# Kernel optimization log

Measured on AMD Instinct MI355X. Metric: run time of the kernel, lower is better.

The kernel has to match this reference:

```python
import jax, jax.numpy as jnp
import numpy as np

B, L, K = 8, 512, 30
F = 128          # node_feat_dim
P = 32           # pair_feat_dim
ED = P + 1       # edge_feat_dim = pair_feat_dim + 1 (rel_dist appended)
NL = 4           # num_layers
H = 128          # hidden_dim


def setup_inputs() -> dict:
    key = jax.random.key(0)
    ks = jax.random.split(key, 14)
    R = jax.random.normal(ks[0], (B, L, 3, 3), dtype=jnp.float32)
    t = jax.random.normal(ks[1], (B, L, 3), dtype=jnp.float32) * 10.0  # spread-out CA coords
    res_feat = jax.random.normal(ks[2], (B, L, F), dtype=jnp.float32)
    pair_feat = jax.random.normal(ks[3], (B, L, L, P), dtype=jnp.float32)
    mask_res = jax.random.bernoulli(ks[4], 0.9, (B, L))
    cin = 2 * F + ED + 1   # coord_net input dim
    nin = F + ED           # node_net input dim
    u = lambda k_, shp, fan: jax.random.uniform(k_, shp, jnp.float32, -1.0 / np.sqrt(fan), 1.0 / np.sqrt(fan))
    return {
        "R": R, "t": t, "res_feat": res_feat, "pair_feat": pair_feat, "mask_res": mask_res,
        "coord_w1": u(ks[5], (NL, cin, H), cin), "coord_b1": u(ks[6], (NL, H), cin),
        "coord_w2": u(ks[7], (NL, H, 1), H),    "coord_b2": u(ks[8], (NL, 1), H),
        "node_w1": u(ks[9], (NL, nin, H), nin), "node_b1": u(ks[10], (NL, H), nin),
        "node_w2": u(ks[11], (NL, H, F), H),    "node_b2": u(ks[12], (NL, F), H),
    }


def reference(R, t, res_feat, pair_feat, mask_res,
              coord_w1, coord_b1, coord_w2, coord_b2,
              node_w1, node_b1, node_w2, node_b2):
    Bv, Lv = mask_res.shape
    pos3 = t.reshape(Bv, Lv, 3)

    # --- KNN graph per batch element (k nearest, no self-loops) ---
    sq = jnp.sum(pos3 * pos3, axis=-1)                                   # [B,L]
    d2 = sq[:, :, None] + sq[:, None, :] - 2.0 * jnp.einsum('bid,bjd->bij', pos3, pos3)
    d2 = d2 + jnp.eye(Lv, dtype=d2.dtype) * 1e10                          # exclude self-loop
    _, nbr_local = jax.lax.top_k(-d2, K)                                  # [B,L,K] neighbor (src) indices per center (dst)
    nbr_global = (nbr_local + (jnp.arange(Bv) * Lv)[:, None, None]).reshape(Bv * Lv, K)

    # --- fixed edge attributes: pair_feat[b, src, dst] ++ initial rel_dist ---
    bi = jnp.arange(Bv)[:, None, None]
    ci = jnp.arange(Lv)[None, :, None]
    epf = pair_feat[bi, nbr_local, ci].reshape(Bv * Lv, K, P)             # [N,K,P]
    pflat = pos3.reshape(-1, 3)
    rel0 = pflat[nbr_global] - pflat[:, None, :]
    dist0 = jnp.linalg.norm(rel0, axis=-1, keepdims=True)                 # [N,K,1]
    edge_attr = jnp.concatenate([epf, dist0], axis=-1)                    # [N,K,ED]

    # constant degree K per node => scatter_mean(dst) == mean over K axis
    agg_edge = edge_attr.mean(axis=1)                                     # [N,ED]
    mflat = mask_res.reshape(-1)
    valid = (mflat[nbr_global] & mflat[:, None]).astype(edge_attr.dtype)[..., None]  # [N,K,1]

    x = res_feat.reshape(Bv * Lv, -1)
    p = pflat
    for l in range(coord_w1.shape[0]):
        rel = p[:, None, :] - p[nbr_global]                               # pos[dst]-pos[src], [N,K,3]
        rd = jnp.linalg.norm(rel, axis=-1, keepdims=True)
        xs = x[nbr_global]                                                # x[src]
        xd = jnp.broadcast_to(x[:, None, :], xs.shape)                    # x[dst]
        cf = jnp.concatenate([xs, xd, edge_attr, rd], axis=-1)            # [N,K,2F+ED+1]
        h = jax.nn.relu(cf @ coord_w1[l] + coord_b1[l])
        w = h @ coord_w2[l] + coord_b2[l]                                 # [N,K,1]
        p = p + (w * rel * valid).mean(axis=1)                            # scatter_mean of delta_coord
        nf = jnp.concatenate([x, agg_edge], axis=-1)
        x = jax.nn.relu(nf @ node_w1[l] + node_b1[l]) @ node_w2[l] + node_b2[l]
    return x.reshape(Bv, Lv, -1)
```

## Files before the change

kernel.cpp:

```cpp
#include <hip/hip_runtime.h>
#include <math.h>

#define LSEQ 512
#define KNN 30
#define NNODES 4096

__device__ float g_agg[NNODES * 33];

__device__ __forceinline__ unsigned long long shfl_xor_u64(unsigned long long v, int m) {
  unsigned lo = (unsigned)__shfl_xor((int)(unsigned)(v & 0xFFFFFFFFull), m, 64);
  unsigned hi = (unsigned)__shfl_xor((int)(unsigned)(v >> 32), m, 64);
  return ((unsigned long long)hi << 32) | lo;
}

__global__ __launch_bounds__(256) void knn_agg_kernel(
    const float* __restrict__ t, const float* __restrict__ pair_feat) {
  __shared__ float sx[LSEQ], sy[LSEQ], sz[LSEQ], sq[LSEQ];
  __shared__ int nbr[4][KNN];
  const int blk = blockIdx.x;
  const int tid = threadIdx.x;
  const int b = blk >> 7;
  for (int j = tid; j < LSEQ; j += 256) {
    float x = t[(b * LSEQ + j) * 3 + 0];
    float y = t[(b * LSEQ + j) * 3 + 1];
    float z = t[(b * LSEQ + j) * 3 + 2];
    sx[j] = x; sy[j] = y; sz[j] = z;
    sq[j] = x * x + y * y + z * z;
  }
  __syncthreads();
  const int w = tid >> 6;
  const int lane = tid & 63;
  const int i = blk * 4 + w;
  const int il = i & (LSEQ - 1);
  const float xi = sx[il], yi = sy[il], zi = sz[il], sqi = sq[il];

  unsigned long long k64[8];
#pragma unroll
  for (int m = 0; m < 8; ++m) {
    int j = lane + 64 * m;
    float d2 = sqi + sq[j] - 2.0f * (xi * sx[j] + yi * sy[j] + zi * sz[j]);
    if (j == il) d2 = 1e30f;
    unsigned u = __float_as_uint(d2);
    u = (u & 0x80000000u) ? ~u : (u | 0x80000000u);
    k64[m] = ((unsigned long long)u << 32) | (unsigned)j;
  }
  unsigned long long lbest = k64[0];
#pragma unroll
  for (int m = 1; m < 8; ++m) lbest = (k64[m] < lbest) ? k64[m] : lbest;

  for (int it = 0; it < KNN; ++it) {
    unsigned long long v = lbest;
#pragma unroll
    for (int off = 32; off >= 1; off >>= 1) {
      unsigned long long o = shfl_xor_u64(v, off);
      v = (o < v) ? o : v;
    }
    int jwin = (int)(v & 0xFFFFFFFFull);
    if (lane == it) nbr[w][it] = jwin;
    if ((jwin & 63) == lane) {
      k64[jwin >> 6] = ~0ull;
      lbest = k64[0];
#pragma unroll
      for (int m = 1; m < 8; ++m) lbest = (k64[m] < lbest) ? k64[m] : lbest;
    }
  }

  float acc = 0.0f;
  const int half = lane >> 5;
  const int c = lane & 31;
  const int base_b = b * LSEQ;
#pragma unroll
  for (int itr = 0; itr < KNN / 2; ++itr) {
    int k = itr * 2 + half;
    int j = nbr[w][k];
    acc += pair_feat[((base_b + j) * LSEQ + il) * 32 + c];
  }
  float other = __shfl_xor(acc, 32, 64);
  float tot = acc + other;
  if (lane < 32) g_agg[i * 33 + c] = tot * (1.0f / KNN);

  float dval = 0.0f;
  if (lane < KNN) {
    int j = nbr[w][lane];
    float dx = xi - sx[j], dy = yi - sy[j], dz = zi - sz[j];
    dval = sqrtf(dx * dx + dy * dy + dz * dz);
  }
#pragma unroll
  for (int off = 32; off >= 1; off >>= 1) dval += __shfl_xor(dval, off, 64);
  if (lane == 0) g_agg[i * 33 + 32] = dval * (1.0f / KNN);
}

#define MT 16
#define NFS 196
#define HS 132
#define WSS 132

__global__ __launch_bounds__(256) void node_mlp_kernel(
    const float* __restrict__ res_feat,
    const float* __restrict__ w1, const float* __restrict__ b1,
    const float* __restrict__ w2, const float* __restrict__ b2,
    float* __restrict__ out) {
  __shared__ float nf[MT * NFS];
  __shared__ float hb[MT * HS];
  __shared__ float wbuf[32 * WSS];
  const int tid = threadIdx.x;
  const int node0 = blockIdx.x * MT;
  const int tx = tid & 31, ty = tid >> 5;
  const int c0 = tx * 4, r0 = ty * 2;

#pragma unroll
  for (int q = 0; q < 2; ++q) {
    int f4 = tid + 256 * q;
    int r = f4 >> 5, c4 = f4 & 31;
    *(float4*)&nf[r * NFS + c4 * 4] =
        *(const float4*)&res_feat[(node0 + r) * 128 + c4 * 4];
  }
  for (int idx = tid; idx < MT * 33; idx += 256) {
    int r = idx / 33, cc = idx - r * 33;
    nf[r * NFS + 128 + cc] = g_agg[(node0 + r) * 33 + cc];
  }
  for (int idx = tid; idx < MT * 31; idx += 256) {
    int r = idx / 31, cc = idx - r * 31;
    nf[r * NFS + 161 + cc] = 0.0f;
  }
  __syncthreads();

  for (int l = 0; l < 4; ++l) {
    const float* W1 = w1 + l * 161 * 128;
    float4 acc[2];
    float4 bin = *(const float4*)&b1[l * 128 + c0];
#pragma unroll
    for (int ii = 0; ii < 2; ++ii) acc[ii] = bin;
    for (int kc = 0; kc < 6; ++kc) {
      __syncthreads();
#pragma unroll
      for (int q = 0; q < 4; ++q) {
        int f4 = tid + 256 * q;
        int kk = f4 >> 5, c4 = f4 & 31;
        int row = kc * 32 + kk;
        row = row > 160 ? 160 : row;
        *(float4*)&wbuf[kk * WSS + c4 * 4] = *(const float4*)&W1[row * 128 + c4 * 4];
      }
      __syncthreads();
#pragma unroll
      for (int k4 = 0; k4 < 8; ++k4) {
        float4 av[2], wv[4];
#pragma unroll
        for (int ii = 0; ii < 2; ++ii)
          av[ii] = *(const float4*)&nf[(r0 + ii) * NFS + kc * 32 + k4 * 4];
#pragma unroll
        for (int q = 0; q < 4; ++q)
          wv[q] = *(const float4*)&wbuf[(k4 * 4 + q) * WSS + c0];
#pragma unroll
        for (int ii = 0; ii < 2; ++ii) {
          const float* ap = (const float*)&av[ii];
#pragma unroll
          for (int q = 0; q < 4; ++q) {
            acc[ii].x = fmaf(ap[q], wv[q].x, acc[ii].x);
            acc[ii].y = fmaf(ap[q], wv[q].y, acc[ii].y);
            acc[ii].z = fmaf(ap[q], wv[q].z, acc[ii].z);
            acc[ii].w = fmaf(ap[q], wv[q].w, acc[ii].w);
          }
        }
      }
    }
#pragma unroll
    for (int ii = 0; ii < 2; ++ii) {
      float4 v = acc[ii];
      v.x = fmaxf(v.x, 0.0f); v.y = fmaxf(v.y, 0.0f);
      v.z = fmaxf(v.z, 0.0f); v.w = fmaxf(v.w, 0.0f);
      *(float4*)&hb[(r0 + ii) * HS + c0] = v;
    }

    const float* W2 = w2 + l * 128 * 128;
    float4 acc2[2];
    float4 bin2 = *(const float4*)&b2[l * 128 + c0];
#pragma unroll
    for (int ii = 0; ii < 2; ++ii) acc2[ii] = bin2;
    for (int kc = 0; kc < 4; ++kc) {
      __syncthreads();
#pragma unroll
      for (int q = 0; q < 4; ++q) {
        int f4 = tid + 256 * q;
        int kk = f4 >> 5, c4 = f4 & 31;
        int row = kc * 32 + kk;
        *(float4*)&wbuf[kk * WSS + c4 * 4] = *(const float4*)&W2[row * 128 + c4 * 4];
      }
      __syncthreads();
#pragma unroll
      for (int k4 = 0; k4 < 8; ++k4) {
        float4 av[2], wv[4];
#pragma unroll
        for (int ii = 0; ii < 2; ++ii)
          av[ii] = *(const float4*)&hb[(r0 + ii) * HS + kc * 32 + k4 * 4];
#pragma unroll
        for (int q = 0; q < 4; ++q)
          wv[q] = *(const float4*)&wbuf[(k4 * 4 + q) * WSS + c0];
#pragma unroll
        for (int ii = 0; ii < 2; ++ii) {
          const float* ap = (const float*)&av[ii];
#pragma unroll
          for (int q = 0; q < 4; ++q) {
            acc2[ii].x = fmaf(ap[q], wv[q].x, acc2[ii].x);
            acc2[ii].y = fmaf(ap[q], wv[q].y, acc2[ii].y);
            acc2[ii].z = fmaf(ap[q], wv[q].z, acc2[ii].z);
            acc2[ii].w = fmaf(ap[q], wv[q].w, acc2[ii].w);
          }
        }
      }
    }
    if (l < 3) {
#pragma unroll
      for (int ii = 0; ii < 2; ++ii)
        *(float4*)&nf[(r0 + ii) * NFS + c0] = acc2[ii];
    } else {
#pragma unroll
      for (int ii = 0; ii < 2; ++ii)
        *(float4*)&out[(node0 + r0 + ii) * 128 + c0] = acc2[ii];
    }
  }
}

extern "C" void kernel_launch(void* const* d_in, const int* in_sizes, int n_in,
                              void* d_out, int out_size, void* d_ws, size_t ws_size,
                              hipStream_t stream) {
  const float* t         = (const float*)d_in[1];
  const float* res_feat  = (const float*)d_in[2];
  const float* pair_feat = (const float*)d_in[3];
  const float* nw1       = (const float*)d_in[9];
  const float* nb1       = (const float*)d_in[10];
  const float* nw2       = (const float*)d_in[11];
  const float* nb2       = (const float*)d_in[12];
  float* out = (float*)d_out;
  (void)in_sizes; (void)n_in; (void)out_size; (void)d_ws; (void)ws_size;

  knn_agg_kernel<<<1024, 256, 0, stream>>>(t, pair_feat);
  node_mlp_kernel<<<NNODES / MT, 256, 0, stream>>>(res_feat, nw1, nb1, nw2, nb2, out);
}
```

Baseline: 419.8 us.

## Use DPP wave reduction in KNN and prefetch weight chunks in node MLP

The KNN argmin reduction swaps the xor-shuffle butterfly for DPP row shifts plus row_bcast, then reads the result from lane 63. The node MLP drops to 128 threads with 4 rows per thread. It register-prefetches the next 32-row weight chunk across both layers' GEMMs, and handles weight row 160 with a separate fma instead of a padded sixth chunk. This aims to cut reduction latency, global-load stalls and wasted padded work, at the cost of more registers and fewer threads per block.

```diff
diff --git a/kernel.cpp b/kernel.cpp
--- a/kernel.cpp
+++ b/kernel.cpp
@@ -7,10 +7,14 @@
 
 __device__ float g_agg[NNODES * 33];
 
-__device__ __forceinline__ unsigned long long shfl_xor_u64(unsigned long long v, int m) {
-  unsigned lo = (unsigned)__shfl_xor((int)(unsigned)(v & 0xFFFFFFFFull), m, 64);
-  unsigned hi = (unsigned)__shfl_xor((int)(unsigned)(v >> 32), m, 64);
-  return ((unsigned long long)hi << 32) | lo;
+template <int CTRL>
+__device__ __forceinline__ unsigned long long dpp_min(unsigned long long v) {
+  int lo = (int)(unsigned)(v & 0xFFFFFFFFull);
+  int hi = (int)(unsigned)(v >> 32);
+  int plo = __builtin_amdgcn_update_dpp(lo, lo, CTRL, 0xF, 0xF, false);
+  int phi = __builtin_amdgcn_update_dpp(hi, hi, CTRL, 0xF, 0xF, false);
+  unsigned long long o = ((unsigned long long)(unsigned)phi << 32) | (unsigned)plo;
+  return (o < v) ? o : v;
 }
 
 __global__ __launch_bounds__(256) void knn_agg_kernel(
@@ -50,13 +54,14 @@
 
   for (int it = 0; it < KNN; ++it) {
     unsigned long long v = lbest;
-#pragma unroll
-    for (int off = 32; off >= 1; off >>= 1) {
-      unsigned long long o = shfl_xor_u64(v, off);
-      v = (o < v) ? o : v;
-    }
-    int jwin = (int)(v & 0xFFFFFFFFull);
-    if (lane == it) nbr[w][it] = jwin;
+    v = dpp_min<0x111>(v);
+    v = dpp_min<0x112>(v);
+    v = dpp_min<0x114>(v);
+    v = dpp_min<0x118>(v);
+    v = dpp_min<0x142>(v);
+    v = dpp_min<0x143>(v);
+    int jwin = __builtin_amdgcn_readlane((int)(unsigned)(v & 0xFFFFFFFFull), 63);
+    if (lane == 0) nbr[w][it] = jwin;
     if ((jwin & 63) == lane) {
       k64[jwin >> 6] = ~0ull;
       lbest = k64[0];
@@ -91,11 +96,12 @@
 }
 
 #define MT 16
-#define NFS 196
+#define NFS 164
 #define HS 132
 #define WSS 132
-
-__global__ __launch_bounds__(256) void node_mlp_kernel(
+#define NCHUNK 36
+
+__global__ __launch_bounds__(128) void node_mlp_kernel(
     const float* __restrict__ res_feat,
     const float* __restrict__ w1, const float* __restrict__ b1,
     const float* __restrict__ w2, const float* __restrict__ b2,
@@ -106,53 +112,72 @@
   const int tid = threadIdx.x;
   const int node0 = blockIdx.x * MT;
   const int tx = tid & 31, ty = tid >> 5;
-  const int c0 = tx * 4, r0 = ty * 2;
-
-#pragma unroll
-  for (int q = 0; q < 2; ++q) {
-    int f4 = tid + 256 * q;
+  const int c0 = tx * 4, r0 = ty * 4;
+
+#pragma unroll
+  for (int q = 0; q < 4; ++q) {
+    int f4 = tid + 128 * q;
     int r = f4 >> 5, c4 = f4 & 31;
     *(float4*)&nf[r * NFS + c4 * 4] =
         *(const float4*)&res_feat[(node0 + r) * 128 + c4 * 4];
   }
-  for (int idx = tid; idx < MT * 33; idx += 256) {
+  for (int idx = tid; idx < MT * 33; idx += 128) {
     int r = idx / 33, cc = idx - r * 33;
     nf[r * NFS + 128 + cc] = g_agg[(node0 + r) * 33 + cc];
   }
-  for (int idx = tid; idx < MT * 31; idx += 256) {
-    int r = idx / 31, cc = idx - r * 31;
-    nf[r * NFS + 161 + cc] = 0.0f;
-  }
-  __syncthreads();
-
+
+  auto chunk_ptr = [&](int g) -> const float* {
+    int l = g / 9, r = g - l * 9;
+    return (r < 5) ? (w1 + (l * 161 + r * 32) * 128)
+                   : (w2 + (l * 128 + (r - 5) * 32) * 128);
+  };
+  float4 pre[8];
+  {
+    const float* cp = chunk_ptr(0);
+#pragma unroll
+    for (int q = 0; q < 8; ++q) {
+      int f4 = tid + 128 * q;
+      pre[q] = *(const float4*)&cp[(f4 >> 5) * 128 + (f4 & 31) * 4];
+    }
+  }
+
+  int g = 0;
   for (int l = 0; l < 4; ++l) {
-    const float* W1 = w1 + l * 161 * 128;
-    float4 acc[2];
-    float4 bin = *(const float4*)&b1[l * 128 + c0];
-#pragma unroll
-    for (int ii = 0; ii < 2; ++ii) acc[ii] = bin;
-    for (int kc = 0; kc < 6; ++kc) {
-      __syncthreads();
-#pragma unroll
-      for (int q = 0; q < 4; ++q) {
-        int f4 = tid + 256 * q;
-        int kk = f4 >> 5, c4 = f4 & 31;
-        int row = kc * 32 + kk;
-        row = row > 160 ? 160 : row;
-        *(float4*)&wbuf[kk * WSS + c4 * 4] = *(const float4*)&W1[row * 128 + c4 * 4];
+    float4 w160 = *(const float4*)&w1[(l * 161 + 160) * 128 + c0];
+
+    float4 acc[4];
+    {
+      float4 bin = *(const float4*)&b1[l * 128 + c0];
+#pragma unroll
+      for (int ii = 0; ii < 4; ++ii) acc[ii] = bin;
+    }
+    for (int kc = 0; kc < 5; ++kc, ++g) {
+      __syncthreads();
+#pragma unroll
+      for (int q = 0; q < 8; ++q) {
+        int f4 = tid + 128 * q;
+        *(float4*)&wbuf[(f4 >> 5) * WSS + (f4 & 31) * 4] = pre[q];
+      }
+      if (g + 1 < NCHUNK) {
+        const float* cp = chunk_ptr(g + 1);
+#pragma unroll
+        for (int q = 0; q < 8; ++q) {
+          int f4 = tid + 128 * q;
+          pre[q] = *(const float4*)&cp[(f4 >> 5) * 128 + (f4 & 31) * 4];
+        }
       }
       __syncthreads();
 #pragma unroll
       for (int k4 = 0; k4 < 8; ++k4) {
-        float4 av[2], wv[4];
-#pragma unroll
-        for (int ii = 0; ii < 2; ++ii)
+        float4 av[4], wv[4];
+#pragma unroll
+        for (int ii = 0; ii < 4; ++ii)
           av[ii] = *(const float4*)&nf[(r0 + ii) * NFS + kc * 32 + k4 * 4];
 #pragma unroll
         for (int q = 0; q < 4; ++q)
           wv[q] = *(const float4*)&wbuf[(k4 * 4 + q) * WSS + c0];
 #pragma unroll
-        for (int ii = 0; ii < 2; ++ii) {
+        for (int ii = 0; ii < 4; ++ii) {
           const float* ap = (const float*)&av[ii];
 #pragma unroll
           for (int q = 0; q < 4; ++q) {
@@ -165,39 +190,49 @@
       }
     }
 #pragma unroll
-    for (int ii = 0; ii < 2; ++ii) {
+    for (int ii = 0; ii < 4; ++ii) {
+      float a160 = nf[(r0 + ii) * NFS + 160];
       float4 v = acc[ii];
-      v.x = fmaxf(v.x, 0.0f); v.y = fmaxf(v.y, 0.0f);
-      v.z = fmaxf(v.z, 0.0f); v.w = fmaxf(v.w, 0.0f);
+      v.x = fmaxf(fmaf(a160, w160.x, v.x), 0.0f);
+      v.y = fmaxf(fmaf(a160, w160.y, v.y), 0.0f);
+      v.z = fmaxf(fmaf(a160, w160.z, v.z), 0.0f);
+      v.w = fmaxf(fmaf(a160, w160.w, v.w), 0.0f);
       *(float4*)&hb[(r0 + ii) * HS + c0] = v;
     }
 
-    const float* W2 = w2 + l * 128 * 128;
-    float4 acc2[2];
-    float4 bin2 = *(const float4*)&b2[l * 128 + c0];
-#pragma unroll
-    for (int ii = 0; ii < 2; ++ii) acc2[ii] = bin2;
-    for (int kc = 0; kc < 4; ++kc) {
-      __syncthreads();
-#pragma unroll
-      for (int q = 0; q < 4; ++q) {
-        int f4 = tid + 256 * q;
-        int kk = f4 >> 5, c4 = f4 & 31;
-        int row = kc * 32 + kk;
-        *(float4*)&wbuf[kk * WSS + c4 * 4] = *(const float4*)&W2[row * 128 + c4 * 4];
+    float4 acc2[4];
+    {
+      float4 bin2 = *(const float4*)&b2[l * 128 + c0];
+#pragma unroll
+      for (int ii = 0; ii < 4; ++ii) acc2[ii] = bin2;
+    }
+    for (int kc = 0; kc < 4; ++kc, ++g) {
+      __syncthreads();
+#pragma unroll
+      for (int q = 0; q < 8; ++q) {
+        int f4 = tid + 128 * q;
+        *(float4*)&wbuf[(f4 >> 5) * WSS + (f4 & 31) * 4] = pre[q];
+      }
+      if (g + 1 < NCHUNK) {
+        const float* cp = chunk_ptr(g + 1);
+#pragma unroll
+        for (int q = 0; q < 8; ++q) {
+          int f4 = tid + 128 * q;
+          pre[q] = *(const float4*)&cp[(f4 >> 5) * 128 + (f4 & 31) * 4];
+        }
       }
       __syncthreads();
 #pragma unroll
       for (int k4 = 0; k4 < 8; ++k4) {
-        float4 av[2], wv[4];
-#pragma unroll
-        for (int ii = 0; ii < 2; ++ii)
+        float4 av[4], wv[4];
+#pragma unroll
+        for (int ii = 0; ii < 4; ++ii)
           av[ii] = *(const float4*)&hb[(r0 + ii) * HS + kc * 32 + k4 * 4];
 #pragma unroll
         for (int q = 0; q < 4; ++q)
           wv[q] = *(const float4*)&wbuf[(k4 * 4 + q) * WSS + c0];
 #pragma unroll
-        for (int ii = 0; ii < 2; ++ii) {
+        for (int ii = 0; ii < 4; ++ii) {
           const float* ap = (const float*)&av[ii];
 #pragma unroll
           for (int q = 0; q < 4; ++q) {
@@ -211,11 +246,11 @@
     }
     if (l < 3) {
 #pragma unroll
-      for (int ii = 0; ii < 2; ++ii)
+      for (int ii = 0; ii < 4; ++ii)
         *(float4*)&nf[(r0 + ii) * NFS + c0] = acc2[ii];
     } else {
 #pragma unroll
-      for (int ii = 0; ii < 2; ++ii)
+      for (int ii = 0; ii < 4; ++ii)
         *(float4*)&out[(node0 + r0 + ii) * 128 + c0] = acc2[ii];
     }
   }
@@ -235,5 +270,5 @@
   (void)in_sizes; (void)n_in; (void)out_size; (void)d_ws; (void)ws_size;
 
   knn_agg_kernel<<<1024, 256, 0, stream>>>(t, pair_feat);
-  node_mlp_kernel<<<NNODES / MT, 256, 0, stream>>>(res_feat, nw1, nb1, nw2, nb2, out);
-}
+  node_mlp_kernel<<<NNODES / MT, 128, 0, stream>>>(res_feat, nw1, nb1, nw2, nb2, out);
+}
```

Result: faster. 411.2 us (-2.0%).
